# Optimization experiments

Hardware: AMD Instinct MI355X
Metric: run time of the kernel (lower is better)

## Reference

```python
import jax, jax.numpy as jnp
import numpy as np

G = 4      # deformable groups
K = 9      # 3x3 kernel points
EPS = 1e-5


def _bilinear_gather(value, loc_y, loc_x):
    # value: (N,H,W,G,Cg); loc_*: (N,H,W,G,K) float pixel coords, zero padding outside.
    N, H, W, g, Cg = value.shape
    y0f = jnp.floor(loc_y); x0f = jnp.floor(loc_x)
    wy = loc_y - y0f; wx = loc_x - x0f
    y0 = y0f.astype(jnp.int32); x0 = x0f.astype(jnp.int32)
    n_idx = jnp.arange(N).reshape(N, 1, 1, 1, 1)
    g_idx = jnp.arange(g).reshape(1, 1, 1, g, 1)

    def corner(yi, xi, w):
        valid = (yi >= 0) & (yi < H) & (xi >= 0) & (xi < W)
        yc = jnp.clip(yi, 0, H - 1); xc = jnp.clip(xi, 0, W - 1)
        v = value[n_idx, yc, xc, g_idx]  # (N,H,W,G,K,Cg) irregular gather
        return v * (w * valid)[..., None]

    return (corner(y0, x0, (1 - wy) * (1 - wx))
            + corner(y0, x0 + 1, (1 - wy) * wx)
            + corner(y0 + 1, x0, wy * (1 - wx))
            + corner(y0 + 1, x0 + 1, wy * wx))


def _dcnv4(t, H, W, Wv, bv, Wom, bom, Wo):
    # DCNv4 on (N,L,C): value proj -> learned-offset bilinear sampling with
    # UNNORMALIZED dynamic weights (no softmax, DCNv4) -> output proj (no bias).
    N, L, C = t.shape
    Cg = C // G
    value = (t @ Wv + bv).reshape(N, H, W, G, Cg)
    om = (t @ Wom + bom).reshape(N, H, W, G, 3 * K)
    offset = om[..., :2 * K].reshape(N, H, W, G, K, 2)  # (dx, dy) per point
    mask = om[..., 2 * K:]                               # (N,H,W,G,K)
    ky, kx = jnp.meshgrid(jnp.arange(-1, 2), jnp.arange(-1, 2), indexing='ij')
    ky = ky.reshape(-1).astype(t.dtype); kx = kx.reshape(-1).astype(t.dtype)
    ys = jnp.arange(H, dtype=t.dtype).reshape(1, H, 1, 1, 1)
    xs = jnp.arange(W, dtype=t.dtype).reshape(1, 1, W, 1, 1)
    loc_y = ys + ky + offset[..., 1]  # (N,H,W,G,K)
    loc_x = xs + kx + offset[..., 0]
    sampled = _bilinear_gather(value, loc_y, loc_x)  # (N,H,W,G,K,Cg)
    out = (sampled * mask[..., None]).sum(axis=4)    # (N,H,W,G,Cg)
    return out.reshape(N, L, C) @ Wo


def _bn(x, gamma, beta):
    # training-mode BatchNorm2d: per-channel batch stats over (N,H,W)
    mean = x.mean(axis=(0, 2, 3), keepdims=True)
    var = ((x - mean) ** 2).mean(axis=(0, 2, 3), keepdims=True)
    return (x - mean) * jax.lax.rsqrt(var + EPS) * gamma.reshape(1, -1, 1, 1) \
        + beta.reshape(1, -1, 1, 1)


def setup_inputs() -> dict:
    key = jax.random.key(0)
    ks = jax.random.split(key, 6)
    N, C, H, W = 4, 128, 64, 64
    s = 1.0 / np.sqrt(C)
    x = jax.random.normal(ks[0], (N, C, H, W), jnp.float32)
    Wv = jax.random.normal(ks[1], (C, C), jnp.float32) * s      # value_proj
    bv = jnp.zeros((C,), jnp.float32)
    Wom = jax.random.normal(ks[2], (C, G * 3 * K), jnp.float32) * 0.01  # offset+mask head
    bom = jnp.zeros((G * 3 * K,), jnp.float32)
    Wo = jax.random.normal(ks[3], (C, C), jnp.float32) * s      # output_proj (bias=False)
    gamma = jnp.ones((C,), jnp.float32)
    beta = jnp.zeros((C,), jnp.float32)
    Wc = jax.random.normal(ks[4], (C, C), jnp.float32) * s      # 1x1 conv (out=in=C)
    return {"x": x, "Wv": Wv, "bv": bv, "Wom": Wom, "bom": bom,
            "Wo": Wo, "gamma": gamma, "beta": beta, "Wc": Wc}


def reference(x, Wv, bv, Wom, bom, Wo, gamma, beta, Wc):
    N, C, H, W = x.shape
    shortcut = x
    t = x.transpose(0, 2, 3, 1).reshape(N, H * W, C)
    t = _dcnv4(t, H, W, Wv, bv, Wom, bom, Wo)
    y = t.reshape(N, H, W, C).transpose(0, 3, 1, 2)
    y = jax.nn.relu(_bn(y, gamma, beta))
    t = y.transpose(0, 2, 3, 1).reshape(N, H * W, C)
    t = _dcnv4(t, H, W, Wv, bv, Wom, bom, Wo)  # same DCNv4 weights reused
    y = t.reshape(N, H, W, C).transpose(0, 3, 1, 2)
    y = _bn(y, gamma, beta)                    # same BN params reused, no relu here
    y = y + shortcut                           # in_channels == out_channels
    return jnp.einsum('nchw,oc->nohw', y, Wc)  # final 1x1 conv
```

## Files before the change

### kernel.cpp

```cpp
#include <hip/hip_runtime.h>
#include <math.h>

#define CC   128
#define NL   16384
#define LHW  4096
#define OMP  112
#define HH   64
#define WW   64

typedef __attribute__((ext_vector_type(8))) short short8;
typedef __attribute__((ext_vector_type(4))) float f32x4;

__device__ __forceinline__ unsigned short f2bf(float f) {
    union { float f; unsigned u; } v; v.f = f;
    unsigned r = v.u + 0x7fff + ((v.u >> 16) & 1);
    return (unsigned short)(r >> 16);
}
__device__ __forceinline__ float bf2f(unsigned short u) {
    union { unsigned u; float f; } v; v.u = ((unsigned)u) << 16;
    return v.f;
}

__global__ __launch_bounds__(256) void prep_kernel(
    const float* __restrict__ Wv, const float* __restrict__ Wom,
    const float* __restrict__ Wo, const float* __restrict__ Wc,
    unsigned short* __restrict__ Wcomb, unsigned short* __restrict__ WoT,
    unsigned short* __restrict__ Wcb, float* __restrict__ stats)
{
    int tid = threadIdx.x;
    if (blockIdx.x == 0) {
        stats[tid] = 0.0f;
        stats[256 + tid] = 0.0f;
    }
    int i = blockIdx.x * 256 + tid;
    if (i < 16384) {
        int n = i >> 7, k = i & 127;
        Wcomb[i] = f2bf(Wv[k * CC + n]);
    } else if (i < 30720) {
        int j = i - 16384; int n = j >> 7, k = j & 127;
        Wcomb[16384 + j] = (n < 108) ? f2bf(Wom[k * 108 + n]) : (unsigned short)0;
    } else if (i < 47104) {
        int j = i - 30720; int n = j >> 7, k = j & 127;
        WoT[j] = f2bf(Wo[k * CC + n]);
    } else if (i < 63488) {
        int j = i - 47104;
        Wcb[j] = f2bf(Wc[j]);
    }
}

template<int IN_MODE>
__global__ __launch_bounds__(256) void gemm_vom_kernel(
    const float* __restrict__ Ain, const unsigned short* __restrict__ Wcomb,
    const float* __restrict__ bv, const float* __restrict__ bom,
    const float* __restrict__ stats, const float* __restrict__ gamma,
    const float* __restrict__ beta,
    unsigned short* __restrict__ val, float* __restrict__ omb)
{
    __shared__ unsigned short As[64 * 136];
    __shared__ unsigned short Bs[240 * 136];
    __shared__ float bnsc[128], bnsh[128];

    int tid = threadIdx.x;
    int block_m = blockIdx.x * 64;

    if (IN_MODE == 1 && tid < 128) {
        const float inv = 1.0f / 16384.0f;
        float mean = stats[tid] * inv;
        float var  = stats[128 + tid] * inv - mean * mean;
        float sc   = rsqrtf(var + 1e-5f) * gamma[tid];
        bnsc[tid] = sc;
        bnsh[tid] = beta[tid] - mean * sc;
    }

#pragma unroll
    for (int i = 0; i < 15; i++) {
        int id = tid + i * 256;
        int r = id >> 4, kc = id & 15;
        float4 v = *(const float4*)(Wcomb + (size_t)r * CC + kc * 8);
        *(float4*)(&Bs[r * 136 + kc * 8]) = v;
    }

    if (IN_MODE == 0) {
        int n   = block_m >> 12;
        int hw0 = block_m & 4095;
#pragma unroll
        for (int i = 0; i < 8; i++) {
            int id = tid + i * 256;
            int c  = id >> 4, j4 = id & 15;
            float4 v = *(const float4*)(Ain + (((size_t)(n * CC + c)) << 12) + hw0 + j4 * 4);
            As[(j4 * 4 + 0) * 136 + c] = f2bf(v.x);
            As[(j4 * 4 + 1) * 136 + c] = f2bf(v.y);
            As[(j4 * 4 + 2) * 136 + c] = f2bf(v.z);
            As[(j4 * 4 + 3) * 136 + c] = f2bf(v.w);
        }
    } else {
        __syncthreads();
#pragma unroll
        for (int i = 0; i < 8; i++) {
            int id = tid + i * 256;
            int r  = id >> 5, c4 = id & 31;
            float4 v = *(const float4*)(Ain + (size_t)(block_m + r) * CC + c4 * 4);
            int c = c4 * 4;
            float a0 = fmaxf(v.x * bnsc[c + 0] + bnsh[c + 0], 0.0f);
            float a1 = fmaxf(v.y * bnsc[c + 1] + bnsh[c + 1], 0.0f);
            float a2 = fmaxf(v.z * bnsc[c + 2] + bnsh[c + 2], 0.0f);
            float a3 = fmaxf(v.w * bnsc[c + 3] + bnsh[c + 3], 0.0f);
            As[r * 136 + c + 0] = f2bf(a0);
            As[r * 136 + c + 1] = f2bf(a1);
            As[r * 136 + c + 2] = f2bf(a2);
            As[r * 136 + c + 3] = f2bf(a3);
        }
    }
    __syncthreads();

    int w  = tid >> 6;
    int l  = tid & 63;
    int lr = l & 15, lk = l >> 4;

    f32x4 acc[15];
#pragma unroll
    for (int nt = 0; nt < 15; nt++) acc[nt] = (f32x4){0.f, 0.f, 0.f, 0.f};

#pragma unroll
    for (int kk = 0; kk < 4; kk++) {
        short8 a = *(const short8*)(&As[(w * 16 + lr) * 136 + kk * 32 + lk * 8]);
#pragma unroll
        for (int nt = 0; nt < 15; nt++) {
            short8 b = *(const short8*)(&Bs[(nt * 16 + lr) * 136 + kk * 32 + lk * 8]);
            acc[nt] = __builtin_amdgcn_mfma_f32_16x16x32_bf16(a, b, acc[nt], 0, 0, 0);
        }
    }

    int row0 = block_m + w * 16 + lk * 4;
#pragma unroll
    for (int nt = 0; nt < 8; nt++) {
        int col = nt * 16 + lr;
        float bb = bv[col];
#pragma unroll
        for (int r = 0; r < 4; r++)
            val[(size_t)(row0 + r) * CC + col] = f2bf(acc[nt][r] + bb);
    }
#pragma unroll
    for (int nt = 8; nt < 15; nt++) {
        int col = (nt - 8) * 16 + lr;
        float bb = (col < 108) ? bom[col] : 0.0f;
#pragma unroll
        for (int r = 0; r < 4; r++)
            omb[(size_t)(row0 + r) * OMP + col] = acc[nt][r] + bb;
    }
}

__global__ __launch_bounds__(256) void sample_kernel(
    const unsigned short* __restrict__ val, const float* __restrict__ omb,
    unsigned int* __restrict__ sbuf)
{
    int tid    = threadIdx.x;
    int gid    = blockIdx.x * 256 + tid;
    int unit   = gid >> 4;
    int lane16 = gid & 15;
    int nl = unit >> 2;
    int g  = unit & 3;
    int n  = nl >> 12;
    int hw = nl & 4095;
    int h  = hw >> 6;
    int w  = hw & 63;

    const float* omp = omb + (size_t)nl * OMP + g * 27;
    const unsigned short* vb = val + (((size_t)n) << 19) + g * 32 + lane16 * 2;

    float acc0 = 0.0f, acc1 = 0.0f;
#pragma unroll
    for (int k = 0; k < 9; k++) {
        float ox = omp[2 * k];
        float oy = omp[2 * k + 1];
        float mk = omp[18 + k];
        float ly = (float)(h + k / 3 - 1) + oy;
        float lx = (float)(w + k % 3 - 1) + ox;
        float y0f = floorf(ly), x0f = floorf(lx);
        float wy = ly - y0f, wx = lx - x0f;
        int y0 = (int)y0f, x0 = (int)x0f;

        float v0 = 0.0f, v1 = 0.0f;
#pragma unroll
        for (int cy = 0; cy < 2; cy++) {
#pragma unroll
            for (int cx = 0; cx < 2; cx++) {
                int yi = y0 + cy, xi = x0 + cx;
                float wgt = (cy ? wy : 1.0f - wy) * (cx ? wx : 1.0f - wx);
                bool valid = (yi >= 0) && (yi < HH) && (xi >= 0) && (xi < WW);
                wgt = valid ? wgt : 0.0f;
                int yc = min(max(yi, 0), HH - 1);
                int xc = min(max(xi, 0), WW - 1);
                unsigned int pv = *(const unsigned int*)(vb + (size_t)(yc * WW + xc) * CC);
                v0 += bf2f((unsigned short)(pv & 0xffff)) * wgt;
                v1 += bf2f((unsigned short)(pv >> 16)) * wgt;
            }
        }
        acc0 += mk * v0;
        acc1 += mk * v1;
    }
    unsigned int packed = (unsigned int)f2bf(acc0) | ((unsigned int)f2bf(acc1) << 16);
    sbuf[(size_t)nl * 64 + g * 16 + lane16] = packed;
}

__global__ __launch_bounds__(256) void gemm_o_bn_kernel(
    const unsigned short* __restrict__ A, const unsigned short* __restrict__ Bt,
    float* __restrict__ ybuf, float* __restrict__ stats)
{
    __shared__ unsigned short As[64 * 136];
    __shared__ unsigned short Bs[128 * 136];
    __shared__ float lstat[256];

    int tid = threadIdx.x;
    int block_m = blockIdx.x * 64;
    lstat[tid] = 0.0f;

#pragma unroll
    for (int i = 0; i < 4; i++) {
        int id = tid + i * 256;
        int r = id >> 4, kc = id & 15;
        float4 v = *(const float4*)(A + (size_t)(block_m + r) * CC + kc * 8);
        *(float4*)(&As[r * 136 + kc * 8]) = v;
    }
#pragma unroll
    for (int i = 0; i < 8; i++) {
        int id = tid + i * 256;
        int r = id >> 4, kc = id & 15;
        float4 v = *(const float4*)(Bt + (size_t)r * CC + kc * 8);
        *(float4*)(&Bs[r * 136 + kc * 8]) = v;
    }
    __syncthreads();

    int w  = tid >> 6;
    int l  = tid & 63;
    int wm = w & 1, wn = w >> 1;
    int lr = l & 15, lk = l >> 4;

    f32x4 acc[2][4];
#pragma unroll
    for (int mt = 0; mt < 2; mt++)
#pragma unroll
        for (int nt = 0; nt < 4; nt++) acc[mt][nt] = (f32x4){0.f, 0.f, 0.f, 0.f};

#pragma unroll
    for (int kk = 0; kk < 4; kk++) {
        short8 a[2], b[4];
#pragma unroll
        for (int mt = 0; mt < 2; mt++)
            a[mt] = *(const short8*)(&As[(wm * 32 + mt * 16 + lr) * 136 + kk * 32 + lk * 8]);
#pragma unroll
        for (int nt = 0; nt < 4; nt++)
            b[nt] = *(const short8*)(&Bs[(wn * 64 + nt * 16 + lr) * 136 + kk * 32 + lk * 8]);
#pragma unroll
        for (int mt = 0; mt < 2; mt++)
#pragma unroll
            for (int nt = 0; nt < 4; nt++)
                acc[mt][nt] = __builtin_amdgcn_mfma_f32_16x16x32_bf16(
                    a[mt], b[nt], acc[mt][nt], 0, 0, 0);
    }

#pragma unroll
    for (int nt = 0; nt < 4; nt++) {
        int col = wn * 64 + nt * 16 + lr;
        float s = 0.0f, sq = 0.0f;
#pragma unroll
        for (int mt = 0; mt < 2; mt++) {
            int row0 = block_m + wm * 32 + mt * 16 + lk * 4;
#pragma unroll
            for (int r = 0; r < 4; r++) {
                float v = acc[mt][nt][r];
                ybuf[(size_t)(row0 + r) * CC + col] = v;
                s += v;
                sq += v * v;
            }
        }
        atomicAdd(&lstat[col], s);
        atomicAdd(&lstat[128 + col], sq);
    }
    __syncthreads();
    if (tid < 128) {
        atomicAdd(&stats[tid], lstat[tid]);
        atomicAdd(&stats[128 + tid], lstat[128 + tid]);
    }
}

__global__ __launch_bounds__(256) void gemm_final_kernel(
    const float* __restrict__ ybuf, const float* __restrict__ x,
    const unsigned short* __restrict__ Bt, const float* __restrict__ stats,
    const float* __restrict__ gamma, const float* __restrict__ beta,
    float* __restrict__ out)
{
    __shared__ unsigned short As[64 * 136];
    __shared__ unsigned short Bs[128 * 136];
    __shared__ float Xs[64 * 132];
    __shared__ float bnsc[128], bnsh[128];

    int tid = threadIdx.x;
    int block_m = blockIdx.x * 64;
    int n   = block_m >> 12;
    int hw0 = block_m & 4095;

    if (tid < 128) {
        const float inv = 1.0f / 16384.0f;
        float mean = stats[tid] * inv;
        float var  = stats[128 + tid] * inv - mean * mean;
        float sc   = rsqrtf(var + 1e-5f) * gamma[tid];
        bnsc[tid] = sc;
        bnsh[tid] = beta[tid] - mean * sc;
    }

#pragma unroll
    for (int i = 0; i < 8; i++) {
        int id = tid + i * 256;
        int c  = id >> 4, j4 = id & 15;
        float4 v = *(const float4*)(x + (((size_t)(n * CC + c)) << 12) + hw0 + j4 * 4);
        Xs[(j4 * 4 + 0) * 132 + c] = v.x;
        Xs[(j4 * 4 + 1) * 132 + c] = v.y;
        Xs[(j4 * 4 + 2) * 132 + c] = v.z;
        Xs[(j4 * 4 + 3) * 132 + c] = v.w;
    }
#pragma unroll
    for (int i = 0; i < 8; i++) {
        int id = tid + i * 256;
        int r = id >> 4, kc = id & 15;
        float4 v = *(const float4*)(Bt + (size_t)r * CC + kc * 8);
        *(float4*)(&Bs[r * 136 + kc * 8]) = v;
    }
    __syncthreads();

#pragma unroll
    for (int i = 0; i < 8; i++) {
        int id = tid + i * 256;
        int r  = id >> 5, c4 = id & 31;
        float4 v = *(const float4*)(ybuf + (size_t)(block_m + r) * CC + c4 * 4);
        int c = c4 * 4;
        float a0 = v.x * bnsc[c + 0] + bnsh[c + 0] + Xs[r * 132 + c + 0];
        float a1 = v.y * bnsc[c + 1] + bnsh[c + 1] + Xs[r * 132 + c + 1];
        float a2 = v.z * bnsc[c + 2] + bnsh[c + 2] + Xs[r * 132 + c + 2];
        float a3 = v.w * bnsc[c + 3] + bnsh[c + 3] + Xs[r * 132 + c + 3];
        As[r * 136 + c + 0] = f2bf(a0);
        As[r * 136 + c + 1] = f2bf(a1);
        As[r * 136 + c + 2] = f2bf(a2);
        As[r * 136 + c + 3] = f2bf(a3);
    }
    __syncthreads();

    int w  = tid >> 6;
    int l  = tid & 63;
    int wm = w & 1, wn = w >> 1;
    int lr = l & 15, lk = l >> 4;

    f32x4 acc[2][4];
#pragma unroll
    for (int mt = 0; mt < 2; mt++)
#pragma unroll
        for (int nt = 0; nt < 4; nt++) acc[mt][nt] = (f32x4){0.f, 0.f, 0.f, 0.f};

#pragma unroll
    for (int kk = 0; kk < 4; kk++) {
        short8 a[2], b[4];
#pragma unroll
        for (int mt = 0; mt < 2; mt++)
            a[mt] = *(const short8*)(&As[(wm * 32 + mt * 16 + lr) * 136 + kk * 32 + lk * 8]);
#pragma unroll
        for (int nt = 0; nt < 4; nt++)
            b[nt] = *(const short8*)(&Bs[(wn * 64 + nt * 16 + lr) * 136 + kk * 32 + lk * 8]);
#pragma unroll
        for (int mt = 0; mt < 2; mt++)
#pragma unroll
            for (int nt = 0; nt < 4; nt++)
                acc[mt][nt] = __builtin_amdgcn_mfma_f32_16x16x32_bf16(
                    a[mt], b[nt], acc[mt][nt], 0, 0, 0);
    }

    __syncthreads();
    float* T = (float*)Bs;
#pragma unroll
    for (int mt = 0; mt < 2; mt++) {
        int rloc = wm * 32 + mt * 16 + lk * 4;
#pragma unroll
        for (int nt = 0; nt < 4; nt++) {
            int col = wn * 64 + nt * 16 + lr;
#pragma unroll
            for (int r = 0; r < 4; r++)
                T[col * 68 + rloc + r] = acc[mt][nt][r];
        }
    }
    __syncthreads();
    int o = tid >> 1, half = tid & 1;
    float* op = out + (((size_t)(n * CC + o)) << 12) + hw0 + half * 32;
#pragma unroll
    for (int i = 0; i < 8; i++) {
        float4 v = *(const float4*)(&T[o * 68 + half * 32 + i * 4]);
        *(float4*)(op + i * 4) = v;
    }
}

extern "C" void kernel_launch(void* const* d_in, const int* in_sizes, int n_in,
                              void* d_out, int out_size, void* d_ws, size_t ws_size,
                              hipStream_t stream)
{
    const float* x     = (const float*)d_in[0];
    const float* Wv    = (const float*)d_in[1];
    const float* bv    = (const float*)d_in[2];
    const float* Wom   = (const float*)d_in[3];
    const float* bom   = (const float*)d_in[4];
    const float* Wo    = (const float*)d_in[5];
    const float* gamma = (const float*)d_in[6];
    const float* beta  = (const float*)d_in[7];
    const float* Wc    = (const float*)d_in[8];
    float* out = (float*)d_out;

    char* ws = (char*)d_ws;
    unsigned short* val   = (unsigned short*)ws;   ws += (size_t)NL * CC * 2;
    float*          omb   = (float*)ws;            ws += (size_t)NL * OMP * 4;
    unsigned int*   sbuf  = (unsigned int*)ws;     ws += (size_t)NL * CC * 2;
    float*          ybuf  = (float*)ws;            ws += (size_t)NL * CC * 4;
    unsigned short* Wcomb = (unsigned short*)ws;   ws += 240 * 128 * 2;
    unsigned short* WoT   = (unsigned short*)ws;   ws += 128 * 128 * 2;
    unsigned short* Wcb   = (unsigned short*)ws;   ws += 128 * 128 * 2;
    float*          stats = (float*)ws;            ws += 2048;

    dim3 b256(256);

    prep_kernel<<<248, b256, 0, stream>>>(Wv, Wom, Wo, Wc, Wcomb, WoT, Wcb, stats);

    gemm_vom_kernel<0><<<256, b256, 0, stream>>>(x, Wcomb, bv, bom,
                                                 nullptr, nullptr, nullptr, val, omb);
    sample_kernel<<<4096, b256, 0, stream>>>(val, omb, sbuf);
    gemm_o_bn_kernel<<<256, b256, 0, stream>>>((const unsigned short*)sbuf, WoT, ybuf, stats);

    gemm_vom_kernel<1><<<256, b256, 0, stream>>>(ybuf, Wcomb, bv, bom,
                                                 stats, gamma, beta, val, omb);
    sample_kernel<<<4096, b256, 0, stream>>>(val, omb, sbuf);
    gemm_o_bn_kernel<<<256, b256, 0, stream>>>((const unsigned short*)sbuf, WoT, ybuf, stats + 256);

    gemm_final_kernel<<<256, b256, 0, stream>>>(ybuf, x, Wcb, stats + 256, gamma, beta, out);
}
```

Baseline: 156.7 us.

## Widen GEMM blocks to 512 threads and split output tiles across more waves

The three GEMM kernels now launch 512 threads (8 waves) per block, and the output tile is repartitioned so each wave owns fewer MFMA fragments. The vom GEMM splits its 15 column fragments across two wave columns. The o_bn GEMM halves its M tile to 32 rows and doubles the grid to 512 blocks. The aim is more waves per CU to hide LDS and global latency in these small-K GEMMs, at the cost of lower per-wave reuse of A fragments and more block-level staging overhead.

```diff
diff --git a/kernel.cpp b/kernel.cpp
--- a/kernel.cpp
+++ b/kernel.cpp
@@ -49,15 +49,15 @@
 }
 
 template<int IN_MODE>
-__global__ __launch_bounds__(256) void gemm_vom_kernel(
+__global__ __launch_bounds__(512, 2) void gemm_vom_kernel(
     const float* __restrict__ Ain, const unsigned short* __restrict__ Wcomb,
     const float* __restrict__ bv, const float* __restrict__ bom,
     const float* __restrict__ stats, const float* __restrict__ gamma,
     const float* __restrict__ beta,
     unsigned short* __restrict__ val, float* __restrict__ omb)
 {
-    __shared__ unsigned short As[64 * 136];
-    __shared__ unsigned short Bs[240 * 136];
+    __shared__ alignas(16) unsigned short As[64 * 136];
+    __shared__ alignas(16) unsigned short Bs[240 * 136];
     __shared__ float bnsc[128], bnsh[128];
 
     int tid = threadIdx.x;
@@ -73,19 +73,21 @@
     }
 
 #pragma unroll
-    for (int i = 0; i < 15; i++) {
-        int id = tid + i * 256;
-        int r = id >> 4, kc = id & 15;
-        float4 v = *(const float4*)(Wcomb + (size_t)r * CC + kc * 8);
-        *(float4*)(&Bs[r * 136 + kc * 8]) = v;
+    for (int i = 0; i < 8; i++) {
+        int id = tid + i * 512;
+        if (id < 3840) {
+            int r = id >> 4, kc = id & 15;
+            float4 v = *(const float4*)(Wcomb + (size_t)r * CC + kc * 8);
+            *(float4*)(&Bs[r * 136 + kc * 8]) = v;
+        }
     }
 
     if (IN_MODE == 0) {
         int n   = block_m >> 12;
         int hw0 = block_m & 4095;
 #pragma unroll
-        for (int i = 0; i < 8; i++) {
-            int id = tid + i * 256;
+        for (int i = 0; i < 4; i++) {
+            int id = tid + i * 512;
             int c  = id >> 4, j4 = id & 15;
             float4 v = *(const float4*)(Ain + (((size_t)(n * CC + c)) << 12) + hw0 + j4 * 4);
             As[(j4 * 4 + 0) * 136 + c] = f2bf(v.x);
@@ -96,8 +98,8 @@
     } else {
         __syncthreads();
 #pragma unroll
-        for (int i = 0; i < 8; i++) {
-            int id = tid + i * 256;
+        for (int i = 0; i < 4; i++) {
+            int id = tid + i * 512;
             int r  = id >> 5, c4 = id & 31;
             float4 v = *(const float4*)(Ain + (size_t)(block_m + r) * CC + c4 * 4);
             int c = c4 * 4;
@@ -116,37 +118,46 @@
     int w  = tid >> 6;
     int l  = tid & 63;
     int lr = l & 15, lk = l >> 4;
-
-    f32x4 acc[15];
-#pragma unroll
-    for (int nt = 0; nt < 15; nt++) acc[nt] = (f32x4){0.f, 0.f, 0.f, 0.f};
+    int wrow = w & 3;
+    int wcol = w >> 2;
+    int F  = wcol * 8;
+    int NF = wcol ? 7 : 8;
+
+    f32x4 acc[8];
+#pragma unroll
+    for (int nt = 0; nt < 8; nt++) acc[nt] = (f32x4){0.f, 0.f, 0.f, 0.f};
 
 #pragma unroll
     for (int kk = 0; kk < 4; kk++) {
-        short8 a = *(const short8*)(&As[(w * 16 + lr) * 136 + kk * 32 + lk * 8]);
-#pragma unroll
-        for (int nt = 0; nt < 15; nt++) {
-            short8 b = *(const short8*)(&Bs[(nt * 16 + lr) * 136 + kk * 32 + lk * 8]);
-            acc[nt] = __builtin_amdgcn_mfma_f32_16x16x32_bf16(a, b, acc[nt], 0, 0, 0);
-        }
-    }
-
-    int row0 = block_m + w * 16 + lk * 4;
+        short8 a = *(const short8*)(&As[(wrow * 16 + lr) * 136 + kk * 32 + lk * 8]);
+#pragma unroll
+        for (int nt = 0; nt < 8; nt++) {
+            if (nt < NF) {
+                short8 b = *(const short8*)(&Bs[((F + nt) * 16 + lr) * 136 + kk * 32 + lk * 8]);
+                acc[nt] = __builtin_amdgcn_mfma_f32_16x16x32_bf16(a, b, acc[nt], 0, 0, 0);
+            }
+        }
+    }
+
+    int row0 = block_m + wrow * 16 + lk * 4;
 #pragma unroll
     for (int nt = 0; nt < 8; nt++) {
-        int col = nt * 16 + lr;
-        float bb = bv[col];
-#pragma unroll
-        for (int r = 0; r < 4; r++)
-            val[(size_t)(row0 + r) * CC + col] = f2bf(acc[nt][r] + bb);
-    }
-#pragma unroll
-    for (int nt = 8; nt < 15; nt++) {
-        int col = (nt - 8) * 16 + lr;
-        float bb = (col < 108) ? bom[col] : 0.0f;
-#pragma unroll
-        for (int r = 0; r < 4; r++)
-            omb[(size_t)(row0 + r) * OMP + col] = acc[nt][r] + bb;
+        if (nt < NF) {
+            int frag = F + nt;
+            if (frag < 8) {
+                int col = frag * 16 + lr;
+                float bb = bv[col];
+#pragma unroll
+                for (int r = 0; r < 4; r++)
+                    val[(size_t)(row0 + r) * CC + col] = f2bf(acc[nt][r] + bb);
+            } else {
+                int ocol = (frag - 8) * 16 + lr;
+                float bb = (ocol < 108) ? bom[ocol] : 0.0f;
+#pragma unroll
+                for (int r = 0; r < 4; r++)
+                    omb[(size_t)(row0 + r) * OMP + ocol] = acc[nt][r] + bb;
+            }
+        }
     }
 }
 
@@ -203,28 +214,26 @@
     sbuf[(size_t)nl * 64 + g * 16 + lane16] = packed;
 }
 
-__global__ __launch_bounds__(256) void gemm_o_bn_kernel(
+__global__ __launch_bounds__(512, 4) void gemm_o_bn_kernel(
     const unsigned short* __restrict__ A, const unsigned short* __restrict__ Bt,
     float* __restrict__ ybuf, float* __restrict__ stats)
 {
-    __shared__ unsigned short As[64 * 136];
-    __shared__ unsigned short Bs[128 * 136];
+    __shared__ alignas(16) unsigned short As[32 * 136];
+    __shared__ alignas(16) unsigned short Bs[128 * 136];
     __shared__ float lstat[256];
 
     int tid = threadIdx.x;
-    int block_m = blockIdx.x * 64;
-    lstat[tid] = 0.0f;
-
-#pragma unroll
-    for (int i = 0; i < 4; i++) {
-        int id = tid + i * 256;
-        int r = id >> 4, kc = id & 15;
+    int block_m = blockIdx.x * 32;
+    if (tid < 256) lstat[tid] = 0.0f;
+
+    {
+        int r = tid >> 4, kc = tid & 15;
         float4 v = *(const float4*)(A + (size_t)(block_m + r) * CC + kc * 8);
         *(float4*)(&As[r * 136 + kc * 8]) = v;
     }
 #pragma unroll
-    for (int i = 0; i < 8; i++) {
-        int id = tid + i * 256;
+    for (int i = 0; i < 4; i++) {
+        int id = tid + i * 512;
         int r = id >> 4, kc = id & 15;
         float4 v = *(const float4*)(Bt + (size_t)r * CC + kc * 8);
         *(float4*)(&Bs[r * 136 + kc * 8]) = v;
@@ -233,46 +242,33 @@
 
     int w  = tid >> 6;
     int l  = tid & 63;
-    int wm = w & 1, wn = w >> 1;
     int lr = l & 15, lk = l >> 4;
-
-    f32x4 acc[2][4];
-#pragma unroll
-    for (int mt = 0; mt < 2; mt++)
-#pragma unroll
-        for (int nt = 0; nt < 4; nt++) acc[mt][nt] = (f32x4){0.f, 0.f, 0.f, 0.f};
-
+    int wr = w & 1, wc = w >> 1;
+
+    f32x4 acc[2];
+    acc[0] = (f32x4){0.f, 0.f, 0.f, 0.f};
+    acc[1] = (f32x4){0.f, 0.f, 0.f, 0.f};
 #pragma unroll
     for (int kk = 0; kk < 4; kk++) {
-        short8 a[2], b[4];
-#pragma unroll
-        for (int mt = 0; mt < 2; mt++)
-            a[mt] = *(const short8*)(&As[(wm * 32 + mt * 16 + lr) * 136 + kk * 32 + lk * 8]);
-#pragma unroll
-        for (int nt = 0; nt < 4; nt++)
-            b[nt] = *(const short8*)(&Bs[(wn * 64 + nt * 16 + lr) * 136 + kk * 32 + lk * 8]);
-#pragma unroll
-        for (int mt = 0; mt < 2; mt++)
-#pragma unroll
-            for (int nt = 0; nt < 4; nt++)
-                acc[mt][nt] = __builtin_amdgcn_mfma_f32_16x16x32_bf16(
-                    a[mt], b[nt], acc[mt][nt], 0, 0, 0);
-    }
-
-#pragma unroll
-    for (int nt = 0; nt < 4; nt++) {
-        int col = wn * 64 + nt * 16 + lr;
+        short8 a = *(const short8*)(&As[(wr * 16 + lr) * 136 + kk * 32 + lk * 8]);
+#pragma unroll
+        for (int nt = 0; nt < 2; nt++) {
+            short8 b = *(const short8*)(&Bs[(wc * 32 + nt * 16 + lr) * 136 + kk * 32 + lk * 8]);
+            acc[nt] = __builtin_amdgcn_mfma_f32_16x16x32_bf16(a, b, acc[nt], 0, 0, 0);
+        }
+    }
+
+    int row0 = block_m + wr * 16 + lk * 4;
+#pragma unroll
+    for (int nt = 0; nt < 2; nt++) {
+        int col = wc * 32 + nt * 16 + lr;
         float s = 0.0f, sq = 0.0f;
 #pragma unroll
-        for (int mt = 0; mt < 2; mt++) {
-            int row0 = block_m + wm * 32 + mt * 16 + lk * 4;
-#pragma unroll
-            for (int r = 0; r < 4; r++) {
-                float v = acc[mt][nt][r];
-                ybuf[(size_t)(row0 + r) * CC + col] = v;
-                s += v;
-                sq += v * v;
-            }
+        for (int r = 0; r < 4; r++) {
+            float v = acc[nt][r];
+            ybuf[(size_t)(row0 + r) * CC + col] = v;
+            s += v;
+            sq += v * v;
         }
         atomicAdd(&lstat[col], s);
         atomicAdd(&lstat[128 + col], sq);
@@ -284,15 +280,15 @@
     }
 }
 
-__global__ __launch_bounds__(256) void gemm_final_kernel(
+__global__ __launch_bounds__(512, 2) void gemm_final_kernel(
     const float* __restrict__ ybuf, const float* __restrict__ x,
     const unsigned short* __restrict__ Bt, const float* __restrict__ stats,
     const float* __restrict__ gamma, const float* __restrict__ beta,
     float* __restrict__ out)
 {
-    __shared__ unsigned short As[64 * 136];
-    __shared__ unsigned short Bs[128 * 136];
-    __shared__ float Xs[64 * 132];
+    __shared__ alignas(16) unsigned short As[64 * 136];
+    __shared__ alignas(16) unsigned short Bs[128 * 136];
+    __shared__ alignas(16) float Xs[64 * 132];
     __shared__ float bnsc[128], bnsh[128];
 
     int tid = threadIdx.x;
@@ -310,8 +306,8 @@
     }
 
 #pragma unroll
-    for (int i = 0; i < 8; i++) {
-        int id = tid + i * 256;
+    for (int i = 0; i < 4; i++) {
+        int id = tid + i * 512;
         int c  = id >> 4, j4 = id & 15;
         float4 v = *(const float4*)(x + (((size_t)(n * CC + c)) << 12) + hw0 + j4 * 4);
         Xs[(j4 * 4 + 0) * 132 + c] = v.x;
@@ -320,8 +316,8 @@
         Xs[(j4 * 4 + 3) * 132 + c] = v.w;
     }
 #pragma unroll
-    for (int i = 0; i < 8; i++) {
-        int id = tid + i * 256;
+    for (int i = 0; i < 4; i++) {
+        int id = tid + i * 512;
         int r = id >> 4, kc = id & 15;
         float4 v = *(const float4*)(Bt + (size_t)r * CC + kc * 8);
         *(float4*)(&Bs[r * 136 + kc * 8]) = v;
@@ -329,8 +325,8 @@
     __syncthreads();
 
 #pragma unroll
-    for (int i = 0; i < 8; i++) {
-        int id = tid + i * 256;
+    for (int i = 0; i < 4; i++) {
+        int id = tid + i * 512;
         int r  = id >> 5, c4 = id & 31;
         float4 v = *(const float4*)(ybuf + (size_t)(block_m + r) * CC + c4 * 4);
         int c = c4 * 4;
@@ -347,51 +343,39 @@
 
     int w  = tid >> 6;
     int l  = tid & 63;
-    int wm = w & 1, wn = w >> 1;
     int lr = l & 15, lk = l >> 4;
-
-    f32x4 acc[2][4];
-#pragma unroll
-    for (int mt = 0; mt < 2; mt++)
-#pragma unroll
-        for (int nt = 0; nt < 4; nt++) acc[mt][nt] = (f32x4){0.f, 0.f, 0.f, 0.f};
+    int wr = w & 3, wc = w >> 2;
+
+    f32x4 acc[4];
+#pragma unroll
+    for (int nt = 0; nt < 4; nt++) acc[nt] = (f32x4){0.f, 0.f, 0.f, 0.f};
 
 #pragma unroll
     for (int kk = 0; kk < 4; kk++) {
-        short8 a[2], b[4];
-#pragma unroll
-        for (int mt = 0; mt < 2; mt++)
-            a[mt] = *(const short8*)(&As[(wm * 32 + mt * 16 + lr) * 136 + kk * 32 + lk * 8]);
-#pragma unroll
-        for (int nt = 0; nt < 4; nt++)
-            b[nt] = *(const short8*)(&Bs[(wn * 64 + nt * 16 + lr) * 136 + kk * 32 + lk * 8]);
-#pragma unroll
-        for (int mt = 0; mt < 2; mt++)
-#pragma unroll
-            for (int nt = 0; nt < 4; nt++)
-                acc[mt][nt] = __builtin_amdgcn_mfma_f32_16x16x32_bf16(
-                    a[mt], b[nt], acc[mt][nt], 0, 0, 0);
+        short8 a = *(const short8*)(&As[(wr * 16 + lr) * 136 + kk * 32 + lk * 8]);
+#pragma unroll
+        for (int nt = 0; nt < 4; nt++) {
+            short8 b = *(const short8*)(&Bs[(wc * 64 + nt * 16 + lr) * 136 + kk * 32 + lk * 8]);
+            acc[nt] = __builtin_amdgcn_mfma_f32_16x16x32_bf16(a, b, acc[nt], 0, 0, 0);
+        }
     }
 
     __syncthreads();
     float* T = (float*)Bs;
-#pragma unroll
-    for (int mt = 0; mt < 2; mt++) {
-        int rloc = wm * 32 + mt * 16 + lk * 4;
-#pragma unroll
-        for (int nt = 0; nt < 4; nt++) {
-            int col = wn * 64 + nt * 16 + lr;
-#pragma unroll
-            for (int r = 0; r < 4; r++)
-                T[col * 68 + rloc + r] = acc[mt][nt][r];
-        }
-    }
-    __syncthreads();
-    int o = tid >> 1, half = tid & 1;
-    float* op = out + (((size_t)(n * CC + o)) << 12) + hw0 + half * 32;
-#pragma unroll
-    for (int i = 0; i < 8; i++) {
-        float4 v = *(const float4*)(&T[o * 68 + half * 32 + i * 4]);
+    int rloc = wr * 16 + lk * 4;
+#pragma unroll
+    for (int nt = 0; nt < 4; nt++) {
+        int col = wc * 64 + nt * 16 + lr;
+#pragma unroll
+        for (int r = 0; r < 4; r++)
+            T[col * 68 + rloc + r] = acc[nt][r];
+    }
+    __syncthreads();
+    int o = tid >> 2, q = tid & 3;
+    float* op = out + (((size_t)(n * CC + o)) << 12) + hw0 + q * 16;
+#pragma unroll
+    for (int i = 0; i < 4; i++) {
+        float4 v = *(const float4*)(&T[o * 68 + q * 16 + i * 4]);
         *(float4*)(op + i * 4) = v;
     }
 }
@@ -421,19 +405,19 @@
     unsigned short* Wcb   = (unsigned short*)ws;   ws += 128 * 128 * 2;
     float*          stats = (float*)ws;            ws += 2048;
 
-    dim3 b256(256);
+    dim3 b256(256), b512(512);
 
     prep_kernel<<<248, b256, 0, stream>>>(Wv, Wom, Wo, Wc, Wcomb, WoT, Wcb, stats);
 
-    gemm_vom_kernel<0><<<256, b256, 0, stream>>>(x, Wcomb, bv, bom,
+    gemm_vom_kernel<0><<<256, b512, 0, stream>>>(x, Wcomb, bv, bom,
                                                  nullptr, nullptr, nullptr, val, omb);
     sample_kernel<<<4096, b256, 0, stream>>>(val, omb, sbuf);
-    gemm_o_bn_kernel<<<256, b256, 0, stream>>>((const unsigned short*)sbuf, WoT, ybuf, stats);
-
-    gemm_vom_kernel<1><<<256, b256, 0, stream>>>(ybuf, Wcomb, bv, bom,
+    gemm_o_bn_kernel<<<512, b512, 0, stream>>>((const unsigned short*)sbuf, WoT, ybuf, stats);
+
+    gemm_vom_kernel<1><<<256, b512, 0, stream>>>(ybuf, Wcomb, bv, bom,
                                                  stats, gamma, beta, val, omb);
     sample_kernel<<<4096, b256, 0, stream>>>(val, omb, sbuf);
-    gemm_o_bn_kernel<<<256, b256, 0, stream>>>((const unsigned short*)sbuf, WoT, ybuf, stats + 256);
-
-    gemm_final_kernel<<<256, b256, 0, stream>>>(ybuf, x, Wcb, stats + 256, gamma, beta, out);
-}
+    gemm_o_bn_kernel<<<512, b512, 0, stream>>>((const unsigned short*)sbuf, WoT, ybuf, stats + 256);
+
+    gemm_final_kernel<<<256, b512, 0, stream>>>(ybuf, x, Wcb, stats + 256, gamma, beta, out);
+}
```

Result: slower. 173.0 us (+10.4%).
